# Optimization experiments

Measured on AMD Instinct MI355X. Metric: run time of the kernel, lower is better.

## Reference

```python
import jax, jax.numpy as jnp
import numpy as np

BITS = 4
MAXQ = (1 << BITS) - 1  # 15
GROUPSIZE = 128
IN_F = 8192
OUT_F = 8192
PACK = 32 // BITS  # 8 values per int32


def setup_inputs() -> dict:
    key = jax.random.key(0)
    k_x, k_w, k_z, k_s, k_b = jax.random.split(key, 5)
    groups = IN_F // GROUPSIZE
    x = jax.random.normal(k_x, (4, 32, IN_F), dtype=jnp.float32)
    # bit-packed int32 weight / zeros (random bit patterns are valid quantized data)
    qweight = jax.random.randint(k_w, (IN_F // PACK, OUT_F), 0, 2**31 - 1, dtype=jnp.int32)
    qzeros = jax.random.randint(k_z, (groups, OUT_F // PACK), 0, 2**31 - 1, dtype=jnp.int32)
    scales = (jax.random.uniform(k_s, (groups, OUT_F), dtype=jnp.float32) * 0.01 + 1e-3)
    g_idx = (jnp.arange(IN_F, dtype=jnp.int32) // GROUPSIZE).astype(jnp.int32)
    bias = jax.random.normal(k_b, (OUT_F,), dtype=jnp.float32) * 0.01
    return {"x": x, "qweight": qweight, "qzeros": qzeros, "scales": scales,
            "g_idx": g_idx, "bias": bias}


def _dequant(qweight, qzeros, scales, g_idx):
    shifts = jnp.arange(0, 32, BITS, dtype=jnp.int32)  # [PACK]
    # unpack weights along the input dim: [in/PACK, PACK, out] -> [in, out]
    w = (qweight[:, None, :] >> shifts[None, :, None]) & MAXQ
    w = w.reshape(-1, qweight.shape[1])
    # unpack zeros along the output dim: [groups, out/PACK, PACK] -> [groups, out]
    # GPTQ stores (zero - 1), so add 1 back
    z = ((qzeros[:, :, None] >> shifts[None, None, :]) & MAXQ) + 1
    z = z.reshape(qzeros.shape[0], -1)
    # per-group dequant: W[i, o] = scales[g_idx[i], o] * (w[i, o] - z[g_idx[i], o])
    W = scales[g_idx] * (w.astype(scales.dtype) - z[g_idx].astype(scales.dtype))
    return W  # [in, out]


def reference(x, qweight, qzeros, scales, g_idx, bias):
    W = _dequant(qweight, qzeros, scales, g_idx)
    out = jnp.einsum('bsi,io->bso', x, W) + bias
    return out
```

## Files before the change

kernel.cpp:

```cpp
#include <hip/hip_runtime.h>
#include <hip/hip_bf16.h>
#include <stdint.h>


#define IN_F 8192
#define OUT_F 8192
#define MROWS 128
#define KSPLIT 8
#define KCHUNK (IN_F / KSPLIT)
#define BN 64
#define BK 128

typedef short short8_t __attribute__((ext_vector_type(8)));
typedef float float4_t __attribute__((ext_vector_type(4)));

__device__ __forceinline__ void gl_lds16(const void* g, void* l) {
  auto g1 = (const __attribute__((address_space(1))) unsigned int*)((uintptr_t)g);
  auto l3 = (__attribute__((address_space(3))) unsigned int*)((uintptr_t)l);
  __builtin_amdgcn_global_load_lds(g1, l3, 16, 0, 0);
}

__global__ void cvt_x(const float* __restrict__ x, unsigned short* __restrict__ xb) {
  const int i = (blockIdx.x * 256 + threadIdx.x) * 8;
  float4_t a = *(const float4_t*)(x + i);
  float4_t b = *(const float4_t*)(x + i + 4);
  union { short8_t v; __hip_bfloat162 h[4]; } u;
  u.h[0] = __float22bfloat162_rn(make_float2(a.x, a.y));
  u.h[1] = __float22bfloat162_rn(make_float2(a.z, a.w));
  u.h[2] = __float22bfloat162_rn(make_float2(b.x, b.y));
  u.h[3] = __float22bfloat162_rn(make_float2(b.z, b.w));
  *(short8_t*)(xb + i) = u.v;
}

__global__ void init_out(float* __restrict__ out, const float* __restrict__ bias) {
  const int i = (blockIdx.x * 256 + threadIdx.x) * 4;
  const int o = i & (OUT_F - 1);
  *(float4_t*)(out + i) = *(const float4_t*)(bias + o);
}

__global__ __launch_bounds__(256, 4) void gptq_gemm(
    const unsigned short* __restrict__ xb,
    const int* __restrict__ qweight,
    const int* __restrict__ qzeros,
    const float* __restrict__ scales,
    float* __restrict__ out)
{
  __shared__ unsigned short As[MROWS * BK];

  const int tid  = threadIdx.x;
  const int lane = tid & 63;
  const int l15  = lane & 15;
  const int qtr  = lane >> 4;
  const int wv   = tid >> 6;
  const int wm   = (wv >> 1) * 64;
  const int wn   = (wv & 1) * 32;

  const int o0  = blockIdx.x * BN;
  const int kc0 = blockIdx.y * KCHUNK;

  float4_t acc[4][2];
  const float4_t z4 = {0.f, 0.f, 0.f, 0.f};
#pragma unroll
  for (int i = 0; i < 4; ++i)
#pragma unroll
    for (int j = 0; j < 2; ++j) acc[i][j] = z4;

#pragma unroll 2
  for (int it = 0; it < KCHUNK / BK; ++it) {
    const int k0 = kc0 + it * BK;
    const int g  = k0 >> 7;

    int qw[4][2];
    const int kp0 = k0 >> 3;
#pragma unroll
    for (int ks = 0; ks < 4; ++ks)
#pragma unroll
      for (int nt = 0; nt < 2; ++nt)
        qw[ks][nt] = qweight[(size_t)(kp0 + ks * 4 + qtr) * OUT_F + o0 + wn + nt * 16 + l15];

    float sc[2]; int zq[2];
#pragma unroll
    for (int nt = 0; nt < 2; ++nt) {
      const int o = o0 + wn + nt * 16 + l15;
      sc[nt] = scales[g * OUT_F + o];
      zq[nt] = qzeros[g * (OUT_F / 8) + (o >> 3)];
    }

#pragma unroll
    for (int inst = 0; inst < 8; ++inst) {
      const int m = wv * 32 + inst * 4 + (lane >> 4);
      const int kb = (lane & 15) ^ (m & 15);
      gl_lds16(xb + (size_t)m * IN_F + k0 + kb * 8,
               (void*)(As + (wv * 32 + inst * 4) * BK));
    }

    __syncthreads();

    float zb[2];
#pragma unroll
    for (int nt = 0; nt < 2; ++nt) {
      const int o = o0 + wn + nt * 16 + l15;
      const int z = ((zq[nt] >> (4 * (o & 7))) & 15) + 1;
      zb[nt] = -sc[nt] * (float)z;
    }

#pragma unroll
    for (int ks = 0; ks < 4; ++ks) {
      const int c = ks * 4 + qtr;
      const int pos8 = (c ^ l15) * 8;

      short8_t af[4];
#pragma unroll
      for (int t = 0; t < 4; ++t)
        af[t] = *(const short8_t*)(As + (wm + t * 16 + l15) * BK + pos8);

      short8_t bf[2];
#pragma unroll
      for (int nt = 0; nt < 2; ++nt) {
        union { short8_t v; __hip_bfloat162 h[4]; } bw;
        const int q = qw[ks][nt];
        const unsigned qe = (unsigned)q & 0x0F0F0F0Fu;
        const unsigned qo = ((unsigned)q >> 4) & 0x0F0F0F0Fu;
#pragma unroll
        for (int jj = 0; jj < 4; ++jj) {
          const float f0 = (float)((qe >> (8 * jj)) & 0xffu);
          const float f1 = (float)((qo >> (8 * jj)) & 0xffu);
          bw.h[jj] = __float22bfloat162_rn(make_float2(
              fmaf(sc[nt], f0, zb[nt]), fmaf(sc[nt], f1, zb[nt])));
        }
        bf[nt] = bw.v;
      }

#pragma unroll
      for (int mt = 0; mt < 4; ++mt)
#pragma unroll
        for (int nt = 0; nt < 2; ++nt)
          acc[mt][nt] = __builtin_amdgcn_mfma_f32_16x16x32_bf16(
              af[mt], bf[nt], acc[mt][nt], 0, 0, 0);
    }

    __syncthreads();
  }

  const int row4 = (lane >> 4) * 4;
#pragma unroll
  for (int mt = 0; mt < 4; ++mt)
#pragma unroll
    for (int nt = 0; nt < 2; ++nt)
#pragma unroll
      for (int rr = 0; rr < 4; ++rr) {
        const int m = wm + mt * 16 + row4 + rr;
        const int o = o0 + wn + nt * 16 + l15;
        atomicAdd(out + (size_t)m * OUT_F + o, acc[mt][nt][rr]);
      }
}

extern "C" void kernel_launch(void* const* d_in, const int* in_sizes, int n_in,
                              void* d_out, int out_size, void* d_ws, size_t ws_size,
                              hipStream_t stream) {
  const float* x        = (const float*)d_in[0];
  const int*   qweight  = (const int*)d_in[1];
  const int*   qzeros   = (const int*)d_in[2];
  const float* scales   = (const float*)d_in[3];
  const float* bias     = (const float*)d_in[5];
  float* out = (float*)d_out;
  unsigned short* xb = (unsigned short*)d_ws;

  cvt_x<<<dim3((MROWS * IN_F) / (256 * 8)), 256, 0, stream>>>(x, xb);
  init_out<<<dim3((MROWS * OUT_F) / (256 * 4)), 256, 0, stream>>>(out, bias);
  gptq_gemm<<<dim3(OUT_F / BN, KSPLIT), 256, 0, stream>>>(xb, qweight, qzeros, scales, out);
}
```

Measured before the change: 128.1 us.

## Replace split-K atomic accumulation with workspace partials and a reduction kernel

When the workspace is large enough, each K-split block writes its partial tile to its own slice of the workspace with plain stores. A separate reduce kernel then sums the eight slices and adds the bias. This removes the float atomics to the output and the bias-init kernel. In exchange it writes and reads about 32 MB of partials and adds one more launch; if the workspace is too small, the old atomic path is used.

```diff
diff --git a/kernel.cpp b/kernel.cpp
--- a/kernel.cpp
+++ b/kernel.cpp
@@ -38,12 +38,24 @@
   *(float4_t*)(out + i) = *(const float4_t*)(bias + o);
 }
 
+__global__ void reduce_out(const float* __restrict__ part, const float* __restrict__ bias,
+                           float* __restrict__ out) {
+  const int i = (blockIdx.x * 256 + threadIdx.x) * 4;
+  const int o = i & (OUT_F - 1);
+  float4_t s = *(const float4_t*)(bias + o);
+#pragma unroll
+  for (int sl = 0; sl < KSPLIT; ++sl)
+    s += *(const float4_t*)(part + (size_t)sl * MROWS * OUT_F + i);
+  *(float4_t*)(out + i) = s;
+}
+
+template <bool USE_WS>
 __global__ __launch_bounds__(256, 4) void gptq_gemm(
     const unsigned short* __restrict__ xb,
     const int* __restrict__ qweight,
     const int* __restrict__ qzeros,
     const float* __restrict__ scales,
-    float* __restrict__ out)
+    float* __restrict__ dst)
 {
   __shared__ unsigned short As[MROWS * BK];
 
@@ -143,6 +155,7 @@
   }
 
   const int row4 = (lane >> 4) * 4;
+  float* base = USE_WS ? (dst + (size_t)blockIdx.y * (MROWS * OUT_F)) : dst;
 #pragma unroll
   for (int mt = 0; mt < 4; ++mt)
 #pragma unroll
@@ -151,7 +164,10 @@
       for (int rr = 0; rr < 4; ++rr) {
         const int m = wm + mt * 16 + row4 + rr;
         const int o = o0 + wn + nt * 16 + l15;
-        atomicAdd(out + (size_t)m * OUT_F + o, acc[mt][nt][rr]);
+        if (USE_WS)
+          base[(size_t)m * OUT_F + o] = acc[mt][nt][rr];
+        else
+          atomicAdd(base + (size_t)m * OUT_F + o, acc[mt][nt][rr]);
       }
 }
 
@@ -164,9 +180,20 @@
   const float* scales   = (const float*)d_in[3];
   const float* bias     = (const float*)d_in[5];
   float* out = (float*)d_out;
+
   unsigned short* xb = (unsigned short*)d_ws;
+  float* part = (float*)((char*)d_ws + (size_t)2 * 1024 * 1024);
+  const size_t need = (size_t)2 * 1024 * 1024 + (size_t)KSPLIT * MROWS * OUT_F * 4;
 
   cvt_x<<<dim3((MROWS * IN_F) / (256 * 8)), 256, 0, stream>>>(x, xb);
-  init_out<<<dim3((MROWS * OUT_F) / (256 * 4)), 256, 0, stream>>>(out, bias);
-  gptq_gemm<<<dim3(OUT_F / BN, KSPLIT), 256, 0, stream>>>(xb, qweight, qzeros, scales, out);
+
+  if (ws_size >= need) {
+    gptq_gemm<true><<<dim3(OUT_F / BN, KSPLIT), 256, 0, stream>>>(
+        xb, qweight, qzeros, scales, part);
+    reduce_out<<<dim3((MROWS * OUT_F) / (256 * 4)), 256, 0, stream>>>(part, bias, out);
+  } else {
+    init_out<<<dim3((MROWS * OUT_F) / (256 * 4)), 256, 0, stream>>>(out, bias);
+    gptq_gemm<false><<<dim3(OUT_F / BN, KSPLIT), 256, 0, stream>>>(
+        xb, qweight, qzeros, scales, out);
+  }
 }
```

Result: faster. 125.4 us (-2.1%).

## Switch to 32x32 MFMA with register-prefetched weights and split-K partial buffer reduction

Applied to the files above, without the earlier changes.

Removes the LDS staging of activations and loads A fragments directly from global memory. Widens the block to BN=128 using 32x32x16 MFMA tiles. Double-buffers the packed weights, scales and zeros in registers to overlap loads with dequant. Replaces float atomics into the output with plain stores to per-split partial buffers, then adds bias in a separate reduction kernel. In exchange it adds 32 MB of partial-buffer traffic, lowers occupancy through launch bounds, and A reuse now depends on the cache rather than shared memory.

```diff
diff --git a/kernel.cpp b/kernel.cpp
--- a/kernel.cpp
+++ b/kernel.cpp
@@ -8,17 +8,11 @@
 #define MROWS 128
 #define KSPLIT 8
 #define KCHUNK (IN_F / KSPLIT)
-#define BN 64
-#define BK 128
+#define BN 128
 
 typedef short short8_t __attribute__((ext_vector_type(8)));
 typedef float float4_t __attribute__((ext_vector_type(4)));
-
-__device__ __forceinline__ void gl_lds16(const void* g, void* l) {
-  auto g1 = (const __attribute__((address_space(1))) unsigned int*)((uintptr_t)g);
-  auto l3 = (__attribute__((address_space(3))) unsigned int*)((uintptr_t)l);
-  __builtin_amdgcn_global_load_lds(g1, l3, 16, 0, 0);
-}
+typedef float float16_t __attribute__((ext_vector_type(16)));
 
 __global__ void cvt_x(const float* __restrict__ x, unsigned short* __restrict__ xb) {
   const int i = (blockIdx.x * 256 + threadIdx.x) * 8;
@@ -32,126 +26,136 @@
   *(short8_t*)(xb + i) = u.v;
 }
 
-__global__ void init_out(float* __restrict__ out, const float* __restrict__ bias) {
+__global__ void reduce_out(const float* __restrict__ part, const float* __restrict__ bias,
+                           float* __restrict__ out) {
   const int i = (blockIdx.x * 256 + threadIdx.x) * 4;
   const int o = i & (OUT_F - 1);
-  *(float4_t*)(out + i) = *(const float4_t*)(bias + o);
+  float4_t s = *(const float4_t*)(bias + o);
+#pragma unroll
+  for (int sl = 0; sl < KSPLIT; ++sl)
+    s += *(const float4_t*)(part + (size_t)sl * MROWS * OUT_F + i);
+  *(float4_t*)(out + i) = s;
 }
 
-__global__ __launch_bounds__(256, 4) void gptq_gemm(
+__global__ __launch_bounds__(256, 2) void gptq_gemm(
     const unsigned short* __restrict__ xb,
     const int* __restrict__ qweight,
     const int* __restrict__ qzeros,
     const float* __restrict__ scales,
-    float* __restrict__ out)
+    float* __restrict__ part)
 {
-  __shared__ unsigned short As[MROWS * BK];
-
   const int tid  = threadIdx.x;
   const int lane = tid & 63;
-  const int l15  = lane & 15;
-  const int qtr  = lane >> 4;
+  const int l31  = lane & 31;
+  const int half = lane >> 5;
   const int wv   = tid >> 6;
   const int wm   = (wv >> 1) * 64;
-  const int wn   = (wv & 1) * 32;
+  const int wn   = (wv & 1) * 64;
 
   const int o0  = blockIdx.x * BN;
   const int kc0 = blockIdx.y * KCHUNK;
+  const int g0  = kc0 >> 7;
+  const int kp_base = (kc0 >> 3) + half;
 
-  float4_t acc[4][2];
-  const float4_t z4 = {0.f, 0.f, 0.f, 0.f};
+  float16_t acc[2][2];
 #pragma unroll
-  for (int i = 0; i < 4; ++i)
+  for (int i = 0; i < 2; ++i)
 #pragma unroll
-    for (int j = 0; j < 2; ++j) acc[i][j] = z4;
+    for (int j = 0; j < 2; ++j)
+#pragma unroll
+      for (int r = 0; r < 16; ++r) acc[i][j][r] = 0.f;
 
-#pragma unroll 2
-  for (int it = 0; it < KCHUNK / BK; ++it) {
-    const int k0 = kc0 + it * BK;
-    const int g  = k0 >> 7;
+  int ocol[2];
+  ocol[0] = o0 + wn + l31;
+  ocol[1] = o0 + wn + 32 + l31;
 
-    int qw[4][2];
-    const int kp0 = k0 >> 3;
-#pragma unroll
-    for (int ks = 0; ks < 4; ++ks)
-#pragma unroll
-      for (int nt = 0; nt < 2; ++nt)
-        qw[ks][nt] = qweight[(size_t)(kp0 + ks * 4 + qtr) * OUT_F + o0 + wn + nt * 16 + l15];
-
-    float sc[2]; int zq[2];
-#pragma unroll
-    for (int nt = 0; nt < 2; ++nt) {
-      const int o = o0 + wn + nt * 16 + l15;
-      sc[nt] = scales[g * OUT_F + o];
-      zq[nt] = qzeros[g * (OUT_F / 8) + (o >> 3)];
-    }
+  int qw[2][8][2];
+  float sc[2][2];
+  int zq[2][2];
 
 #pragma unroll
-    for (int inst = 0; inst < 8; ++inst) {
-      const int m = wv * 32 + inst * 4 + (lane >> 4);
-      const int kb = (lane & 15) ^ (m & 15);
-      gl_lds16(xb + (size_t)m * IN_F + k0 + kb * 8,
-               (void*)(As + (wv * 32 + inst * 4) * BK));
+  for (int ks = 0; ks < 8; ++ks)
+#pragma unroll
+    for (int nt = 0; nt < 2; ++nt)
+      qw[0][ks][nt] = qweight[(size_t)(kp_base + ks * 2) * OUT_F + ocol[nt]];
+#pragma unroll
+  for (int nt = 0; nt < 2; ++nt) {
+    sc[0][nt] = scales[g0 * OUT_F + ocol[nt]];
+    zq[0][nt] = qzeros[g0 * (OUT_F / 8) + (ocol[nt] >> 3)];
+  }
+
+  for (int gi = 0; gi < KCHUNK / 128; ++gi) {
+    const int cur = gi & 1, nxt = cur ^ 1;
+
+    if (gi + 1 < KCHUNK / 128) {
+      const int kp_n = kp_base + (gi + 1) * 16;
+#pragma unroll
+      for (int ks = 0; ks < 8; ++ks)
+#pragma unroll
+        for (int nt = 0; nt < 2; ++nt)
+          qw[nxt][ks][nt] = qweight[(size_t)(kp_n + ks * 2) * OUT_F + ocol[nt]];
+      const int gn = g0 + gi + 1;
+#pragma unroll
+      for (int nt = 0; nt < 2; ++nt) {
+        sc[nxt][nt] = scales[gn * OUT_F + ocol[nt]];
+        zq[nxt][nt] = qzeros[gn * (OUT_F / 8) + (ocol[nt] >> 3)];
+      }
     }
-
-    __syncthreads();
 
     float zb[2];
 #pragma unroll
     for (int nt = 0; nt < 2; ++nt) {
-      const int o = o0 + wn + nt * 16 + l15;
-      const int z = ((zq[nt] >> (4 * (o & 7))) & 15) + 1;
-      zb[nt] = -sc[nt] * (float)z;
+      const int z = ((zq[cur][nt] >> (4 * (ocol[nt] & 7))) & 15) + 1;
+      zb[nt] = -sc[cur][nt] * (float)z;
     }
 
+    const int kg = kc0 + gi * 128;
+
 #pragma unroll
-    for (int ks = 0; ks < 4; ++ks) {
-      const int c = ks * 4 + qtr;
-      const int pos8 = (c ^ l15) * 8;
+    for (int ks = 0; ks < 8; ++ks) {
+      const int k = kg + ks * 16 + half * 8;
 
-      short8_t af[4];
+      short8_t af[2];
 #pragma unroll
-      for (int t = 0; t < 4; ++t)
-        af[t] = *(const short8_t*)(As + (wm + t * 16 + l15) * BK + pos8);
+      for (int mt = 0; mt < 2; ++mt)
+        af[mt] = *(const short8_t*)(xb + (size_t)(wm + mt * 32 + l31) * IN_F + k);
 
       short8_t bf[2];
 #pragma unroll
       for (int nt = 0; nt < 2; ++nt) {
         union { short8_t v; __hip_bfloat162 h[4]; } bw;
-        const int q = qw[ks][nt];
-        const unsigned qe = (unsigned)q & 0x0F0F0F0Fu;
-        const unsigned qo = ((unsigned)q >> 4) & 0x0F0F0F0Fu;
+        const unsigned q = (unsigned)qw[cur][ks][nt];
+        const unsigned qe = q & 0x0F0F0F0Fu;
+        const unsigned qo = (q >> 4) & 0x0F0F0F0Fu;
 #pragma unroll
         for (int jj = 0; jj < 4; ++jj) {
           const float f0 = (float)((qe >> (8 * jj)) & 0xffu);
           const float f1 = (float)((qo >> (8 * jj)) & 0xffu);
           bw.h[jj] = __float22bfloat162_rn(make_float2(
-              fmaf(sc[nt], f0, zb[nt]), fmaf(sc[nt], f1, zb[nt])));
+              fmaf(sc[cur][nt], f0, zb[nt]), fmaf(sc[cur][nt], f1, zb[nt])));
         }
         bf[nt] = bw.v;
       }
 
 #pragma unroll
-      for (int mt = 0; mt < 4; ++mt)
+      for (int mt = 0; mt < 2; ++mt)
 #pragma unroll
         for (int nt = 0; nt < 2; ++nt)
-          acc[mt][nt] = __builtin_amdgcn_mfma_f32_16x16x32_bf16(
+          acc[mt][nt] = __builtin_amdgcn_mfma_f32_32x32x16_bf16(
               af[mt], bf[nt], acc[mt][nt], 0, 0, 0);
     }
-
-    __syncthreads();
   }
 
-  const int row4 = (lane >> 4) * 4;
+  float* base = part + (size_t)blockIdx.y * (MROWS * OUT_F);
 #pragma unroll
-  for (int mt = 0; mt < 4; ++mt)
+  for (int mt = 0; mt < 2; ++mt)
 #pragma unroll
     for (int nt = 0; nt < 2; ++nt)
 #pragma unroll
-      for (int rr = 0; rr < 4; ++rr) {
-        const int m = wm + mt * 16 + row4 + rr;
-        const int o = o0 + wn + nt * 16 + l15;
-        atomicAdd(out + (size_t)m * OUT_F + o, acc[mt][nt][rr]);
+      for (int r = 0; r < 16; ++r) {
+        const int row = (r & 3) + 8 * (r >> 2) + 4 * half;
+        const int m = wm + mt * 32 + row;
+        base[(size_t)m * OUT_F + ocol[nt]] = acc[mt][nt][r];
       }
 }
 
@@ -164,9 +168,11 @@
   const float* scales   = (const float*)d_in[3];
   const float* bias     = (const float*)d_in[5];
   float* out = (float*)d_out;
+
   unsigned short* xb = (unsigned short*)d_ws;
+  float* part = (float*)((char*)d_ws + (size_t)2 * 1024 * 1024);
 
   cvt_x<<<dim3((MROWS * IN_F) / (256 * 8)), 256, 0, stream>>>(x, xb);
-  init_out<<<dim3((MROWS * OUT_F) / (256 * 4)), 256, 0, stream>>>(out, bias);
-  gptq_gemm<<<dim3(OUT_F / BN, KSPLIT), 256, 0, stream>>>(xb, qweight, qzeros, scales, out);
+  gptq_gemm<<<dim3(OUT_F / BN, KSPLIT), 256, 0, stream>>>(xb, qweight, qzeros, scales, part);
+  reduce_out<<<dim3((MROWS * OUT_F) / (256 * 4)), 256, 0, stream>>>(part, bias, out);
 }
```

Measured after the change: 139.8 us. 9.1% more time.

## Double-buffer GEMM loads, halve K-split, replace atomics with partial-sum reduction

Applied to the files above, without the earlier changes.

The main loop now double-buffers the LDS activation tile and the register copies of packed weights, scales and zeros, so the next tile's loads are issued before the current tile's MFMA work. The K split drops from 8 to 4 and launch bounds go from 4 to 2 blocks per CU. Atomic adds to the output are replaced by plain stores into per-slice partial buffers, followed by a separate reduce kernel that adds the slices and the bias. In exchange it needs 16 MB of extra workspace and an extra pass over that memory, and the grid has half as many blocks, which could leave the GPU underfilled.

```diff
diff --git a/kernel.cpp b/kernel.cpp
--- a/kernel.cpp
+++ b/kernel.cpp
@@ -6,10 +6,11 @@
 #define IN_F 8192
 #define OUT_F 8192
 #define MROWS 128
-#define KSPLIT 8
+#define KSPLIT 4
 #define KCHUNK (IN_F / KSPLIT)
 #define BN 64
 #define BK 128
+#define NITER (KCHUNK / BK)
 
 typedef short short8_t __attribute__((ext_vector_type(8)));
 typedef float float4_t __attribute__((ext_vector_type(4)));
@@ -32,20 +33,25 @@
   *(short8_t*)(xb + i) = u.v;
 }
 
-__global__ void init_out(float* __restrict__ out, const float* __restrict__ bias) {
+__global__ void reduce_out(const float* __restrict__ part, const float* __restrict__ bias,
+                           float* __restrict__ out) {
   const int i = (blockIdx.x * 256 + threadIdx.x) * 4;
   const int o = i & (OUT_F - 1);
-  *(float4_t*)(out + i) = *(const float4_t*)(bias + o);
-}
-
-__global__ __launch_bounds__(256, 4) void gptq_gemm(
+  float4_t s = *(const float4_t*)(bias + o);
+#pragma unroll
+  for (int sl = 0; sl < KSPLIT; ++sl)
+    s += *(const float4_t*)(part + (size_t)sl * MROWS * OUT_F + i);
+  *(float4_t*)(out + i) = s;
+}
+
+__global__ __launch_bounds__(256, 2) void gptq_gemm(
     const unsigned short* __restrict__ xb,
     const int* __restrict__ qweight,
     const int* __restrict__ qzeros,
     const float* __restrict__ scales,
-    float* __restrict__ out)
+    float* __restrict__ part)
 {
-  __shared__ unsigned short As[MROWS * BK];
+  __shared__ unsigned short As[2][MROWS * BK];
 
   const int tid  = threadIdx.x;
   const int lane = tid & 63;
@@ -58,6 +64,9 @@
   const int o0  = blockIdx.x * BN;
   const int kc0 = blockIdx.y * KCHUNK;
 
+  const int arow = lane >> 4;
+  const int akb  = lane & 15;
+
   float4_t acc[4][2];
   const float4_t z4 = {0.f, 0.f, 0.f, 0.f};
 #pragma unroll
@@ -65,43 +74,64 @@
 #pragma unroll
     for (int j = 0; j < 2; ++j) acc[i][j] = z4;
 
-#pragma unroll 2
-  for (int it = 0; it < KCHUNK / BK; ++it) {
-    const int k0 = kc0 + it * BK;
-    const int g  = k0 >> 7;
-
-    int qw[4][2];
-    const int kp0 = k0 >> 3;
-#pragma unroll
-    for (int ks = 0; ks < 4; ++ks)
-#pragma unroll
-      for (int nt = 0; nt < 2; ++nt)
-        qw[ks][nt] = qweight[(size_t)(kp0 + ks * 4 + qtr) * OUT_F + o0 + wn + nt * 16 + l15];
-
-    float sc[2]; int zq[2];
+  int   qw[2][4][2];
+  float sc[2][2];
+  int   zq[2][2];
+
+  const int oc0 = o0 + wn + l15;
+  const int oc1 = oc0 + 16;
+
+  {
+    const int kp0 = kc0 >> 3;
+#pragma unroll
+    for (int ks = 0; ks < 4; ++ks) {
+      qw[0][ks][0] = qweight[(size_t)(kp0 + ks * 4 + qtr) * OUT_F + oc0];
+      qw[0][ks][1] = qweight[(size_t)(kp0 + ks * 4 + qtr) * OUT_F + oc1];
+    }
+    const int g = kc0 >> 7;
+    sc[0][0] = scales[g * OUT_F + oc0];
+    sc[0][1] = scales[g * OUT_F + oc1];
+    zq[0][0] = qzeros[g * (OUT_F / 8) + (oc0 >> 3)];
+    zq[0][1] = qzeros[g * (OUT_F / 8) + (oc1 >> 3)];
+#pragma unroll
+    for (int inst = 0; inst < 8; ++inst) {
+      const int m = wv * 32 + inst * 4 + arow;
+      gl_lds16(xb + (size_t)m * IN_F + kc0 + (akb ^ (m & 15)) * 8,
+               (void*)(As[0] + (wv * 32 + inst * 4) * BK));
+    }
+  }
+  __syncthreads();
+
+  for (int it = 0; it < NITER; ++it) {
+    const int cur = it & 1, nxt = cur ^ 1;
+
+    if (it + 1 < NITER) {
+      const int k1 = kc0 + (it + 1) * BK;
+      const int kp1 = k1 >> 3;
+#pragma unroll
+      for (int ks = 0; ks < 4; ++ks) {
+        qw[nxt][ks][0] = qweight[(size_t)(kp1 + ks * 4 + qtr) * OUT_F + oc0];
+        qw[nxt][ks][1] = qweight[(size_t)(kp1 + ks * 4 + qtr) * OUT_F + oc1];
+      }
+      const int gn = k1 >> 7;
+      sc[nxt][0] = scales[gn * OUT_F + oc0];
+      sc[nxt][1] = scales[gn * OUT_F + oc1];
+      zq[nxt][0] = qzeros[gn * (OUT_F / 8) + (oc0 >> 3)];
+      zq[nxt][1] = qzeros[gn * (OUT_F / 8) + (oc1 >> 3)];
+#pragma unroll
+      for (int inst = 0; inst < 8; ++inst) {
+        const int m = wv * 32 + inst * 4 + arow;
+        gl_lds16(xb + (size_t)m * IN_F + k1 + (akb ^ (m & 15)) * 8,
+                 (void*)(As[nxt] + (wv * 32 + inst * 4) * BK));
+      }
+    }
+
+    float zb[2];
 #pragma unroll
     for (int nt = 0; nt < 2; ++nt) {
-      const int o = o0 + wn + nt * 16 + l15;
-      sc[nt] = scales[g * OUT_F + o];
-      zq[nt] = qzeros[g * (OUT_F / 8) + (o >> 3)];
-    }
-
-#pragma unroll
-    for (int inst = 0; inst < 8; ++inst) {
-      const int m = wv * 32 + inst * 4 + (lane >> 4);
-      const int kb = (lane & 15) ^ (m & 15);
-      gl_lds16(xb + (size_t)m * IN_F + k0 + kb * 8,
-               (void*)(As + (wv * 32 + inst * 4) * BK));
-    }
-
-    __syncthreads();
-
-    float zb[2];
-#pragma unroll
-    for (int nt = 0; nt < 2; ++nt) {
-      const int o = o0 + wn + nt * 16 + l15;
-      const int z = ((zq[nt] >> (4 * (o & 7))) & 15) + 1;
-      zb[nt] = -sc[nt] * (float)z;
+      const int o = (nt ? oc1 : oc0);
+      const int z = ((zq[cur][nt] >> (4 * (o & 7))) & 15) + 1;
+      zb[nt] = -sc[cur][nt] * (float)z;
     }
 
 #pragma unroll
@@ -112,21 +142,21 @@
       short8_t af[4];
 #pragma unroll
       for (int t = 0; t < 4; ++t)
-        af[t] = *(const short8_t*)(As + (wm + t * 16 + l15) * BK + pos8);
+        af[t] = *(const short8_t*)(As[cur] + (wm + t * 16 + l15) * BK + pos8);
 
       short8_t bf[2];
 #pragma unroll
       for (int nt = 0; nt < 2; ++nt) {
         union { short8_t v; __hip_bfloat162 h[4]; } bw;
-        const int q = qw[ks][nt];
-        const unsigned qe = (unsigned)q & 0x0F0F0F0Fu;
-        const unsigned qo = ((unsigned)q >> 4) & 0x0F0F0F0Fu;
+        const unsigned q = (unsigned)qw[cur][ks][nt];
+        const unsigned qe = q & 0x0F0F0F0Fu;
+        const unsigned qo = (q >> 4) & 0x0F0F0F0Fu;
 #pragma unroll
         for (int jj = 0; jj < 4; ++jj) {
           const float f0 = (float)((qe >> (8 * jj)) & 0xffu);
           const float f1 = (float)((qo >> (8 * jj)) & 0xffu);
           bw.h[jj] = __float22bfloat162_rn(make_float2(
-              fmaf(sc[nt], f0, zb[nt]), fmaf(sc[nt], f1, zb[nt])));
+              fmaf(sc[cur][nt], f0, zb[nt]), fmaf(sc[cur][nt], f1, zb[nt])));
         }
         bf[nt] = bw.v;
       }
@@ -143,6 +173,7 @@
   }
 
   const int row4 = (lane >> 4) * 4;
+  float* base = part + (size_t)blockIdx.y * (MROWS * OUT_F);
 #pragma unroll
   for (int mt = 0; mt < 4; ++mt)
 #pragma unroll
@@ -150,8 +181,7 @@
 #pragma unroll
       for (int rr = 0; rr < 4; ++rr) {
         const int m = wm + mt * 16 + row4 + rr;
-        const int o = o0 + wn + nt * 16 + l15;
-        atomicAdd(out + (size_t)m * OUT_F + o, acc[mt][nt][rr]);
+        base[(size_t)m * OUT_F + (nt ? oc1 : oc0)] = acc[mt][nt][rr];
       }
 }
 
@@ -164,9 +194,11 @@
   const float* scales   = (const float*)d_in[3];
   const float* bias     = (const float*)d_in[5];
   float* out = (float*)d_out;
+
   unsigned short* xb = (unsigned short*)d_ws;
+  float* part = (float*)((char*)d_ws + (size_t)2 * 1024 * 1024);
 
   cvt_x<<<dim3((MROWS * IN_F) / (256 * 8)), 256, 0, stream>>>(x, xb);
-  init_out<<<dim3((MROWS * OUT_F) / (256 * 4)), 256, 0, stream>>>(out, bias);
-  gptq_gemm<<<dim3(OUT_F / BN, KSPLIT), 256, 0, stream>>>(xb, qweight, qzeros, scales, out);
-}
+  gptq_gemm<<<dim3(OUT_F / BN, KSPLIT), 256, 0, stream>>>(xb, qweight, qzeros, scales, part);
+  reduce_out<<<dim3((MROWS * OUT_F) / (256 * 4)), 256, 0, stream>>>(part, bias, out);
+}
```

Result: slower. 133.2 us (+4.0%).
